# Optimization experiments

Measured on AMD Instinct MI355X. Metric: run time of the kernel, lower is better.

Reference implementation:

```python
import jax, jax.numpy as jnp
import numpy as np

D_IN = 1024      # points per target cloud
SPACE = 3        # spatial dim
BOTT = 64        # bottleneck size
GP = 4           # grid points per axis -> G = GP**SPACE = 64
BATCH = 2


def _linear_params(key, fan_in, fan_out):
    # torch.nn.Linear default init: U(-1/sqrt(fan_in), 1/sqrt(fan_in))
    lim = 1.0 / np.sqrt(fan_in)
    kw, kb = jax.random.split(key)
    W = jax.random.uniform(kw, (fan_in, fan_out), minval=-lim, maxval=lim, dtype=jnp.float32)
    b = jax.random.uniform(kb, (fan_out,), minval=-lim, maxval=lim, dtype=jnp.float32)
    return W, b


def setup_inputs() -> dict:
    key = jax.random.key(0)
    ks = jax.random.split(key, 8)
    x = jax.random.normal(ks[0], (BATCH, D_IN, SPACE), dtype=jnp.float32)
    # grid of GP**SPACE points in [0,1]^SPACE (np.meshgrid as in the module)
    axes = [np.linspace(0.0, 1.0, GP, dtype=np.float32) for _ in range(SPACE)]
    grid = jnp.asarray(np.stack(np.meshgrid(*axes), axis=-1).reshape(-1, SPACE))  # [G, 3]
    We1, be1 = _linear_params(ks[1], D_IN * SPACE, 512)
    We2, be2 = _linear_params(ks[2], 512, 128)
    We3, be3 = _linear_params(ks[3], 128, BOTT)
    Wd1, bd1 = _linear_params(ks[4], BOTT + SPACE, 128)
    Wd2, bd2 = _linear_params(ks[5], 128, 512)
    Wd3, bd3 = _linear_params(ks[6], 512, D_IN * SPACE)
    return {"x": x, "grid": grid,
            "We1": We1, "be1": be1, "We2": We2, "be2": be2, "We3": We3, "be3": be3,
            "Wd1": Wd1, "bd1": bd1, "Wd2": Wd2, "bd2": bd2, "Wd3": Wd3, "bd3": bd3}


def reference(x, grid, We1, be1, We2, be2, We3, be3, Wd1, bd1, Wd2, bd2, Wd3, bd3):
    B = x.shape[0]
    G = grid.shape[0]
    # encoder: flatten cloud -> latent  [B, BOTT]
    xf = x.reshape(B, -1)
    h = jax.nn.relu(xf @ We1 + be1)
    h = jax.nn.relu(h @ We2 + be2)
    z = jax.nn.relu(h @ We3 + be3)
    # decoder: concat(latent, grid point) for every grid point  [B, G, BOTT+SPACE]
    zi = jnp.concatenate([
        jnp.broadcast_to(z[:, None, :], (B, G, z.shape[-1])),
        jnp.broadcast_to(grid[None, :, :], (B, G, SPACE)),
    ], axis=-1)
    d = jax.nn.relu(zi @ Wd1 + bd1)
    d = jax.nn.relu(d @ Wd2 + bd2)
    d = jnp.tanh(d @ Wd3 + bd3)            # [B, G, D_IN*SPACE]
    Y = d.reshape(B, G * D_IN, SPACE)      # generated point set, N = G*D_IN
    S = x                                  # target point set,   M = D_IN
    # pairwise squared distances [B, N, M] via ||y||^2 + ||s||^2 - 2 y.s
    d2 = ((Y * Y).sum(-1)[:, :, None]
          + (S * S).sum(-1)[:, None, :]
          - 2.0 * jnp.einsum('bnd,bmd->bnm', Y, S))
    # symmetric chamfer: sum of min over each direction
    loss = jnp.sum(jnp.min(d2, axis=2)) + jnp.sum(jnp.min(d2, axis=1))
    return loss
```

## Files before the change

### kernel.cpp

```cpp
#include <hip/hip_runtime.h>

#define NB 2
#define NPTS 1024
#define NGEN 65536

typedef float f32x2 __attribute__((ext_vector_type(2)));

#define OFF_GW    0
#define OFF_H1P   8192
#define OFF_ZW    32768
#define OFF_S4    33280
#define OFF_Y4    41472
#define OFF_WT4   565760
#define OFF_MPART 2138624

__global__ __launch_bounds__(256) void kA_init(
    const float* __restrict__ x, const float* __restrict__ grid,
    const float* __restrict__ Wd1, const float* __restrict__ Wd3,
    const float* __restrict__ We1,
    float* __restrict__ gw, float* __restrict__ S4,
    float4* __restrict__ Wt4, float* __restrict__ h1part) {
  if (blockIdx.x < 64) {
    int t = blockIdx.x * 256 + threadIdx.x;
    if (t < 8192) {
      int g = t >> 7, j = t & 127;
      float a = grid[g * 3 + 0] * Wd1[64 * 128 + j]
              + grid[g * 3 + 1] * Wd1[65 * 128 + j]
              + grid[g * 3 + 2] * Wd1[66 * 128 + j];
      gw[t] = a;
    } else if (t < 10240) {
      int p = t - 8192;
      const float* xp = x + p * 3;
      float s0 = xp[0], s1 = xp[1], s2 = xp[2];
      ((float4*)S4)[p] = make_float4(s0, s1, s2, s0 * s0 + s1 * s1 + s2 * s2);
    }
  } else if (blockIdx.x < 1600) {
    int tid = (blockIdx.x - 64) * 256 + threadIdx.x;
    int p  = tid & 1023;
    int k4 = (tid >> 10) & 127;
    int c  = tid >> 17;
    const float* W = Wd3 + (k4 * 4) * 3072 + p * 3 + c;
    float w0 = W[0], w1 = W[3072], w2 = W[2 * 3072], w3 = W[3 * 3072];
    Wt4[(c * 128 + k4) * 1024 + p] = make_float4(w0, w1, w2, w3);
  } else {
    int idx = blockIdx.x - 1600;
    int kc = idx % 24;
    int rest = idx / 24;
    int jh = rest & 1;
    int b  = rest >> 1;
    int j = jh * 256 + threadIdx.x;
    const float* xb = x + b * 3072 + kc * 128;
    const float* W  = We1 + (kc * 128) * 512 + j;
    float acc = 0.f;
#pragma unroll 8
    for (int k = 0; k < 128; ++k) acc += xb[k] * W[k * 512];
    h1part[kc * 1024 + b * 512 + j] = acc;
  }
}

__global__ __launch_bounds__(512) void kB_enc(
    const float* __restrict__ h1part, const float* __restrict__ be1,
    const float* __restrict__ We2, const float* __restrict__ be2,
    const float* __restrict__ We3, const float* __restrict__ be3,
    const float* __restrict__ Wd1, const float* __restrict__ bd1,
    float* __restrict__ zw, float* __restrict__ out) {
  __shared__ float h1l[512];
  __shared__ float h2p[512];
  __shared__ float h2l[128];
  __shared__ float zp[512];
  __shared__ float zl[64];
  __shared__ float wp[512];
  int b = blockIdx.x;
  int t = threadIdx.x;
  if (b == 0 && t == 0) out[0] = 0.f;
  {
    float a = be1[t];
#pragma unroll
    for (int kc = 0; kc < 24; ++kc) a += h1part[kc * 1024 + b * 512 + t];
    h1l[t] = fmaxf(a, 0.f);
  }
  __syncthreads();
  {
    int q = t >> 7, j = t & 127;
    const float* W = We2 + (q * 128) * 128 + j;
    const float* h = h1l + q * 128;
    float a = 0.f;
#pragma unroll 16
    for (int k = 0; k < 128; ++k) a += h[k] * W[k * 128];
    h2p[t] = a;
  }
  __syncthreads();
  if (t < 128)
    h2l[t] = fmaxf(h2p[t] + h2p[128 + t] + h2p[256 + t] + h2p[384 + t]
                   + be2[t], 0.f);
  __syncthreads();
  {
    int q = t >> 6, j = t & 63;
    float a = 0.f;
#pragma unroll
    for (int kk = 0; kk < 16; ++kk) {
      int k = q * 16 + kk;
      a += h2l[k] * We3[k * 64 + j];
    }
    zp[t] = a;
  }
  __syncthreads();
  if (t < 64) {
    float a = be3[t];
#pragma unroll
    for (int q = 0; q < 8; ++q) a += zp[q * 64 + t];
    zl[t] = fmaxf(a, 0.f);
  }
  __syncthreads();
  {
    int q = t >> 7, j = t & 127;
    float a = 0.f;
#pragma unroll
    for (int kk = 0; kk < 16; ++kk) {
      int k = q * 16 + kk;
      a += zl[k] * Wd1[k * 128 + j];
    }
    wp[t] = a;
  }
  __syncthreads();
  if (t < 128)
    zw[b * 128 + t] = wp[t] + wp[128 + t] + wp[256 + t] + wp[384 + t]
                      + bd1[t];
}

__global__ __launch_bounds__(512) void kC_dec23_y4(
    const float* __restrict__ zw, const float* __restrict__ gw,
    const float* __restrict__ Wd2, const float* __restrict__ bd2,
    const float4* __restrict__ Wt4, const float* __restrict__ bd3,
    float4* __restrict__ Y4) {
  __shared__ float4 a_lds[8 * 128];
  __shared__ float part[8 * 3 * 8 * 64];
  __shared__ float d1l[128 * 8];
  int rt = blockIdx.x >> 4;
  int pg = blockIdx.x & 15;
  int t = threadIdx.x;
#pragma unroll
  for (int i = 0; i < 2; ++i) {
    int idx2 = i * 512 + t;
    int r = idx2 >> 7, kk = idx2 & 127;
    int row = rt * 8 + r, b = row >> 6, g = row & 63;
    d1l[kk * 8 + r] = fmaxf(zw[b * 128 + kk] + gw[g * 128 + kk], 0.f);
  }
  __syncthreads();
  {
    float* a_f = (float*)a_lds;
    int j = t;
    float bj = bd2[j];
    f32x2 acc01 = {bj, bj}, acc23 = {bj, bj};
    f32x2 acc45 = {bj, bj}, acc67 = {bj, bj};
#pragma unroll 8
    for (int k = 0; k < 128; ++k) {
      float wv = Wd2[k * 512 + j];
      f32x2 wv2 = {wv, wv};
      float4 lo = *(const float4*)(d1l + k * 8);
      float4 hi = *(const float4*)(d1l + k * 8 + 4);
      f32x2 d01 = {lo.x, lo.y}, d23 = {lo.z, lo.w};
      f32x2 d45 = {hi.x, hi.y}, d67 = {hi.z, hi.w};
      acc01 = __builtin_elementwise_fma(d01, wv2, acc01);
      acc23 = __builtin_elementwise_fma(d23, wv2, acc23);
      acc45 = __builtin_elementwise_fma(d45, wv2, acc45);
      acc67 = __builtin_elementwise_fma(d67, wv2, acc67);
    }
    a_f[0 * 512 + j] = fmaxf(acc01.x, 0.f);
    a_f[1 * 512 + j] = fmaxf(acc01.y, 0.f);
    a_f[2 * 512 + j] = fmaxf(acc23.x, 0.f);
    a_f[3 * 512 + j] = fmaxf(acc23.y, 0.f);
    a_f[4 * 512 + j] = fmaxf(acc45.x, 0.f);
    a_f[5 * 512 + j] = fmaxf(acc45.y, 0.f);
    a_f[6 * 512 + j] = fmaxf(acc67.x, 0.f);
    a_f[7 * 512 + j] = fmaxf(acc67.y, 0.f);
  }
  __syncthreads();
  int lane = t & 63, w = t >> 6;
  int p = pg * 64 + lane;
  const float4* wp0 = Wt4 + p;
  const float4* wp1 = Wt4 + 131072 + p;
  const float4* wp2 = Wt4 + 262144 + p;
  float acc[8][3];
#pragma unroll
  for (int r = 0; r < 8; ++r)
#pragma unroll
    for (int c = 0; c < 3; ++c) acc[r][c] = 0.f;
  int kbase = w * 16;
#pragma unroll 4
  for (int i = 0; i < 16; ++i) {
    int k4 = kbase + i;
    float4 w0 = wp0[k4 * 1024];
    float4 w1 = wp1[k4 * 1024];
    float4 w2 = wp2[k4 * 1024];
#pragma unroll
    for (int r = 0; r < 8; ++r) {
      float4 A = a_lds[r * 128 + k4];
      acc[r][0] += A.x * w0.x + A.y * w0.y + A.z * w0.z + A.w * w0.w;
      acc[r][1] += A.x * w1.x + A.y * w1.y + A.z * w1.z + A.w * w1.w;
      acc[r][2] += A.x * w2.x + A.y * w2.y + A.z * w2.z + A.w * w2.w;
    }
  }
#pragma unroll
  for (int r = 0; r < 8; ++r)
#pragma unroll
    for (int c = 0; c < 3; ++c)
      part[((r * 3 + c) * 8 + w) * 64 + lane] = acc[r][c];
  __syncthreads();
  {
    int r = w;
    float s0 = 0.f, s1 = 0.f, s2 = 0.f;
#pragma unroll
    for (int ww = 0; ww < 8; ++ww) {
      s0 += part[((r * 3 + 0) * 8 + ww) * 64 + lane];
      s1 += part[((r * 3 + 1) * 8 + ww) * 64 + lane];
      s2 += part[((r * 3 + 2) * 8 + ww) * 64 + lane];
    }
    float b0 = bd3[p * 3], b1 = bd3[p * 3 + 1], b2 = bd3[p * 3 + 2];
    float y0 = tanhf(s0 + b0), y1 = tanhf(s1 + b1), y2 = tanhf(s2 + b2);
    int row = rt * 8 + r;
    Y4[row * 1024 + p] = make_float4(-2.f * y0, -2.f * y1, -2.f * y2,
                                     y0 * y0 + y1 * y1 + y2 * y2);
  }
}

__global__ __launch_bounds__(256) void kD_chamfer(
    const float4* __restrict__ Y4, const float4* __restrict__ S4,
    float* __restrict__ mpart, float* __restrict__ out) {
  __shared__ float4 c_lds[1024];
  int t = threadIdx.x;
  if (blockIdx.x < 256) {
    int b = blockIdx.x >> 7, nt = blockIdx.x & 127;
    {
      const float4* src = S4 + b * 1024;
#pragma unroll
      for (int i = 0; i < 4; ++i) c_lds[i * 256 + t] = src[i * 256 + t];
    }
    float4 my0 = Y4[b * 65536 + nt * 512 + t];
    float4 my1 = Y4[b * 65536 + nt * 512 + 256 + t];
    f32x2 mx2 = {my0.x, my1.x};
    f32x2 my2 = {my0.y, my1.y};
    f32x2 mz2 = {my0.z, my1.z};
    __syncthreads();
    float mn0 = __builtin_inff(), mn1 = mn0;
#pragma unroll 8
    for (int m = 0; m < 1024; ++m) {
      float4 s = c_lds[m];
      f32x2 sx2 = {s.x, s.x}, sy2 = {s.y, s.y};
      f32x2 sz2 = {s.z, s.z}, sw2 = {s.w, s.w};
      f32x2 d = __builtin_elementwise_fma(sz2, mz2, sw2);
      d = __builtin_elementwise_fma(sy2, my2, d);
      d = __builtin_elementwise_fma(sx2, mx2, d);
      mn0 = fminf(mn0, d.x);
      mn1 = fminf(mn1, d.y);
    }
    float v = (mn0 + my0.w) + (mn1 + my1.w);
#pragma unroll
    for (int off = 32; off > 0; off >>= 1) v += __shfl_down(v, off);
    __shared__ float bsum[4];
    int lane = t & 63, w = t >> 6;
    if (lane == 0) bsum[w] = v;
    __syncthreads();
    if (t == 0) atomicAdd(out, bsum[0] + bsum[1] + bsum[2] + bsum[3]);
  } else {
    int blk = blockIdx.x - 256;
    int b   = blk >> 7;
    int mg  = (blk >> 6) & 1;
    int nch = blk & 63;
    {
      const float4* src = Y4 + b * 65536 + nch * 1024;
#pragma unroll
      for (int i = 0; i < 4; ++i) c_lds[i * 256 + t] = src[i * 256 + t];
    }
    float4 s0 = S4[b * 1024 + mg * 512 + t];
    float4 s1 = S4[b * 1024 + mg * 512 + 256 + t];
    f32x2 sx2 = {s0.x, s1.x};
    f32x2 sy2 = {s0.y, s1.y};
    f32x2 sz2 = {s0.z, s1.z};
    __syncthreads();
    float mn0 = __builtin_inff(), mn1 = mn0;
#pragma unroll 8
    for (int n = 0; n < 1024; ++n) {
      float4 y = c_lds[n];
      f32x2 yx2 = {y.x, y.x}, yy2 = {y.y, y.y};
      f32x2 yz2 = {y.z, y.z}, yw2 = {y.w, y.w};
      f32x2 d = __builtin_elementwise_fma(yz2, sz2, yw2);
      d = __builtin_elementwise_fma(yy2, sy2, d);
      d = __builtin_elementwise_fma(yx2, sx2, d);
      mn0 = fminf(mn0, d.x);
      mn1 = fminf(mn1, d.y);
    }
    int base = (nch * 2 + b) * 1024 + mg * 512;
    mpart[base + t]       = mn0 + s0.w;
    mpart[base + 256 + t] = mn1 + s1.w;
  }
}

__global__ __launch_bounds__(256) void kE_dir2_reduce(
    const float* __restrict__ mpart, float* __restrict__ out) {
  int gid = blockIdx.x * 256 + threadIdx.x;
  int b = gid >> 10, m = gid & 1023;
  float v = __builtin_inff();
#pragma unroll 8
  for (int ch = 0; ch < 64; ++ch)
    v = fminf(v, mpart[(ch * 2 + b) * 1024 + m]);
#pragma unroll
  for (int off = 32; off > 0; off >>= 1) v += __shfl_down(v, off);
  __shared__ float bsum[4];
  int lane = threadIdx.x & 63, w = threadIdx.x >> 6;
  if (lane == 0) bsum[w] = v;
  __syncthreads();
  if (threadIdx.x == 0) atomicAdd(out, bsum[0] + bsum[1] + bsum[2] + bsum[3]);
}

extern "C" void kernel_launch(void* const* d_in, const int* in_sizes, int n_in,
                              void* d_out, int out_size, void* d_ws, size_t ws_size,
                              hipStream_t stream) {
  const float* x   = (const float*)d_in[0];
  const float* grd = (const float*)d_in[1];
  const float* We1 = (const float*)d_in[2];
  const float* be1 = (const float*)d_in[3];
  const float* We2 = (const float*)d_in[4];
  const float* be2 = (const float*)d_in[5];
  const float* We3 = (const float*)d_in[6];
  const float* be3 = (const float*)d_in[7];
  const float* Wd1 = (const float*)d_in[8];
  const float* bd1 = (const float*)d_in[9];
  const float* Wd2 = (const float*)d_in[10];
  const float* bd2 = (const float*)d_in[11];
  const float* Wd3 = (const float*)d_in[12];
  const float* bd3 = (const float*)d_in[13];
  float* ws = (float*)d_ws;
  float* out = (float*)d_out;

  float* gw     = ws + OFF_GW;
  float* h1part = ws + OFF_H1P;
  float* zw     = ws + OFF_ZW;
  float* S4     = ws + OFF_S4;
  float* Y4     = ws + OFF_Y4;
  float4* Wt4   = (float4*)(ws + OFF_WT4);
  float* mpart  = ws + OFF_MPART;

  hipLaunchKernelGGL(kA_init, dim3(1696), dim3(256), 0, stream,
                     x, grd, Wd1, Wd3, We1, gw, S4, Wt4, h1part);
  hipLaunchKernelGGL(kB_enc, dim3(2), dim3(512), 0, stream,
                     h1part, be1, We2, be2, We3, be3, Wd1, bd1, zw, out);
  hipLaunchKernelGGL(kC_dec23_y4, dim3(256), dim3(512), 0, stream,
                     zw, gw, Wd2, bd2, Wt4, bd3, (float4*)Y4);
  hipLaunchKernelGGL(kD_chamfer, dim3(512), dim3(256), 0, stream,
                     (const float4*)Y4, (const float4*)S4, mpart, out);
  hipLaunchKernelGGL(kE_dir2_reduce, dim3(8), dim3(256), 0, stream,
                     mpart, out);
}
```

Before: 165.4 us.

## Read Wd3 directly in decoder GEMM instead of pre-transposing into workspace

Removes the per-call pass in kA_init that rearranged Wd3 into an interleaved float4 workspace buffer (about 6 MB read and written). The decoder kernel now loads Wd3 directly with scalar strided loads of 3 contiguous floats per row. Separately, the We1 partial-product blocks now compute both batches per block, which halves that grid. The aim is to cut the transpose traffic and grid size, at the cost of less vectorized, less coalesced weight loads in the main decoder loop.

```diff
diff --git a/kernel.cpp b/kernel.cpp
--- a/kernel.cpp
+++ b/kernel.cpp
@@ -11,15 +11,13 @@
 #define OFF_ZW    32768
 #define OFF_S4    33280
 #define OFF_Y4    41472
-#define OFF_WT4   565760
-#define OFF_MPART 2138624
+#define OFF_MPART 565760
 
 __global__ __launch_bounds__(256) void kA_init(
     const float* __restrict__ x, const float* __restrict__ grid,
-    const float* __restrict__ Wd1, const float* __restrict__ Wd3,
-    const float* __restrict__ We1,
+    const float* __restrict__ Wd1, const float* __restrict__ We1,
     float* __restrict__ gw, float* __restrict__ S4,
-    float4* __restrict__ Wt4, float* __restrict__ h1part) {
+    float* __restrict__ h1part) {
   if (blockIdx.x < 64) {
     int t = blockIdx.x * 256 + threadIdx.x;
     if (t < 8192) {
@@ -34,27 +32,23 @@
       float s0 = xp[0], s1 = xp[1], s2 = xp[2];
       ((float4*)S4)[p] = make_float4(s0, s1, s2, s0 * s0 + s1 * s1 + s2 * s2);
     }
-  } else if (blockIdx.x < 1600) {
-    int tid = (blockIdx.x - 64) * 256 + threadIdx.x;
-    int p  = tid & 1023;
-    int k4 = (tid >> 10) & 127;
-    int c  = tid >> 17;
-    const float* W = Wd3 + (k4 * 4) * 3072 + p * 3 + c;
-    float w0 = W[0], w1 = W[3072], w2 = W[2 * 3072], w3 = W[3 * 3072];
-    Wt4[(c * 128 + k4) * 1024 + p] = make_float4(w0, w1, w2, w3);
   } else {
-    int idx = blockIdx.x - 1600;
+    int idx = blockIdx.x - 64;
     int kc = idx % 24;
-    int rest = idx / 24;
-    int jh = rest & 1;
-    int b  = rest >> 1;
+    int jh = idx / 24;
     int j = jh * 256 + threadIdx.x;
-    const float* xb = x + b * 3072 + kc * 128;
+    const float* xb0 = x + kc * 128;
+    const float* xb1 = x + 3072 + kc * 128;
     const float* W  = We1 + (kc * 128) * 512 + j;
-    float acc = 0.f;
-#pragma unroll 8
-    for (int k = 0; k < 128; ++k) acc += xb[k] * W[k * 512];
-    h1part[kc * 1024 + b * 512 + j] = acc;
+    float acc0 = 0.f, acc1 = 0.f;
+#pragma unroll 16
+    for (int k = 0; k < 128; ++k) {
+      float wv = W[k * 512];
+      acc0 += xb0[k] * wv;
+      acc1 += xb1[k] * wv;
+    }
+    h1part[kc * 1024 + j] = acc0;
+    h1part[kc * 1024 + 512 + j] = acc1;
   }
 }
 
@@ -131,7 +125,7 @@
 __global__ __launch_bounds__(512) void kC_dec23_y4(
     const float* __restrict__ zw, const float* __restrict__ gw,
     const float* __restrict__ Wd2, const float* __restrict__ bd2,
-    const float4* __restrict__ Wt4, const float* __restrict__ bd3,
+    const float* __restrict__ Wd3, const float* __restrict__ bd3,
     float4* __restrict__ Y4) {
   __shared__ float4 a_lds[8 * 128];
   __shared__ float part[8 * 3 * 8 * 64];
@@ -178,9 +172,7 @@
   __syncthreads();
   int lane = t & 63, w = t >> 6;
   int p = pg * 64 + lane;
-  const float4* wp0 = Wt4 + p;
-  const float4* wp1 = Wt4 + 131072 + p;
-  const float4* wp2 = Wt4 + 262144 + p;
+  const float* wbase = Wd3 + 3 * p;
   float acc[8][3];
 #pragma unroll
   for (int r = 0; r < 8; ++r)
@@ -190,15 +182,17 @@
 #pragma unroll 4
   for (int i = 0; i < 16; ++i) {
     int k4 = kbase + i;
-    float4 w0 = wp0[k4 * 1024];
-    float4 w1 = wp1[k4 * 1024];
-    float4 w2 = wp2[k4 * 1024];
+    const float* wr = wbase + (k4 * 4) * 3072;
+    float w00 = wr[0],    w01 = wr[1],    w02 = wr[2];
+    float w10 = wr[3072], w11 = wr[3073], w12 = wr[3074];
+    float w20 = wr[6144], w21 = wr[6145], w22 = wr[6146];
+    float w30 = wr[9216], w31 = wr[9217], w32 = wr[9218];
 #pragma unroll
     for (int r = 0; r < 8; ++r) {
       float4 A = a_lds[r * 128 + k4];
-      acc[r][0] += A.x * w0.x + A.y * w0.y + A.z * w0.z + A.w * w0.w;
-      acc[r][1] += A.x * w1.x + A.y * w1.y + A.z * w1.z + A.w * w1.w;
-      acc[r][2] += A.x * w2.x + A.y * w2.y + A.z * w2.z + A.w * w2.w;
+      acc[r][0] += A.x * w00 + A.y * w10 + A.z * w20 + A.w * w30;
+      acc[r][1] += A.x * w01 + A.y * w11 + A.z * w21 + A.w * w31;
+      acc[r][2] += A.x * w02 + A.y * w12 + A.z * w22 + A.w * w32;
     }
   }
 #pragma unroll
@@ -338,15 +332,14 @@
   float* zw     = ws + OFF_ZW;
   float* S4     = ws + OFF_S4;
   float* Y4     = ws + OFF_Y4;
-  float4* Wt4   = (float4*)(ws + OFF_WT4);
   float* mpart  = ws + OFF_MPART;
 
-  hipLaunchKernelGGL(kA_init, dim3(1696), dim3(256), 0, stream,
-                     x, grd, Wd1, Wd3, We1, gw, S4, Wt4, h1part);
+  hipLaunchKernelGGL(kA_init, dim3(112), dim3(256), 0, stream,
+                     x, grd, Wd1, We1, gw, S4, h1part);
   hipLaunchKernelGGL(kB_enc, dim3(2), dim3(512), 0, stream,
                      h1part, be1, We2, be2, We3, be3, Wd1, bd1, zw, out);
   hipLaunchKernelGGL(kC_dec23_y4, dim3(256), dim3(512), 0, stream,
-                     zw, gw, Wd2, bd2, Wt4, bd3, (float4*)Y4);
+                     zw, gw, Wd2, bd2, Wd3, bd3, (float4*)Y4);
   hipLaunchKernelGGL(kD_chamfer, dim3(512), dim3(256), 0, stream,
                      (const float4*)Y4, (const float4*)S4, mpart, out);
   hipLaunchKernelGGL(kE_dir2_reduce, dim3(8), dim3(256), 0, stream,
```

Result: no change. 163.0 us (-1.4%).
